# Kernel optimization log

Hardware: AMD Instinct MI355X
Metric: run time of the kernel (lower is better)

Reference implementation:

```python
import jax, jax.numpy as jnp
import numpy as np

B, C, IC, H, W = 4, 64, 32, 128, 128


def _conv1x1(x, w, b):
    # x: [b,c,h,w], w: [o,c], b: [o]
    return jnp.einsum('bchw,oc->bohw', x, w) + b[None, :, None, None]


def _maxpool2(x):
    b, c, h, w = x.shape
    return x.reshape(b, c, h // 2, 2, w // 2, 2).max(axis=(3, 5))


def setup_inputs() -> dict:
    key = jax.random.key(0)
    ks = jax.random.split(key, 11)
    sc = 0.05
    return {
        'target': jax.random.normal(ks[0], (B, C, H, W), jnp.float32),
        'ref': jax.random.normal(ks[1], (B, C, H, W), jnp.float32),
        'ref_align': jax.random.normal(ks[2], (B, C, H, W), jnp.float32),
        'theta_w': jax.random.normal(ks[3], (IC, C), jnp.float32) * sc,
        'theta_b': jax.random.normal(ks[4], (IC,), jnp.float32) * sc,
        'phi_w': jax.random.normal(ks[5], (IC, C), jnp.float32) * sc,
        'phi_b': jax.random.normal(ks[6], (IC,), jnp.float32) * sc,
        'g_w': jax.random.normal(ks[7], (IC, C), jnp.float32) * sc,
        'g_b': jax.random.normal(ks[8], (IC,), jnp.float32) * sc,
        'W_w': jax.random.normal(ks[9], (C, IC), jnp.float32) * sc,
        'W_b': jax.random.normal(ks[10], (C,), jnp.float32) * sc,
    }


def reference(target, ref, ref_align, theta_w, theta_b, phi_w, phi_b, g_w, g_b, W_w, W_b):
    b, c, h, w = target.shape
    N = h * w
    # phi, g: 1x1 conv then 2x2 maxpool -> [b, ic, N/4]
    phi = _maxpool2(_conv1x1(ref, phi_w, phi_b)).reshape(b, -1, N // 4)
    g = _maxpool2(_conv1x1(ref_align, g_w, g_b)).reshape(b, -1, N // 4)
    theta = _conv1x1(target, theta_w, theta_b).reshape(b, -1, N)  # [b, ic, N]
    # softmax-free attention: s [b, N, N/4]
    s = jnp.einsum('bin,bim->bnm', theta, phi) / N
    y = jnp.einsum('bnm,bim->bin', s, g)  # [b, ic, N]
    y = y.reshape(b, -1, h, w)
    return _conv1x1(y, W_w, W_b) + target
```

## Files before the change

### kernel.cpp

```cpp
#include <hip/hip_runtime.h>

#define Bn  4
#define Cc  64
#define ICc 32
#define Hh  128
#define Ww  128
#define Nn  (Hh*Ww)
#define Hp  (Hh/2)
#define Wp  (Ww/2)
#define Mm  (Hp*Wp)
#define Sg  4

__global__ __launch_bounds__(256) void conv_pool_kernel(
    const float* __restrict__ ref, const float* __restrict__ ref_align,
    const float* __restrict__ phi_w, const float* __restrict__ phi_b,
    const float* __restrict__ g_w,   const float* __restrict__ g_b,
    float* __restrict__ P, float* __restrict__ G)
{
    const int z   = blockIdx.z;
    const int inp = z & 1;
    const int ich = (z >> 1) * 16;
    const float* in   = inp ? ref_align : ref;
    const float* wmat = (inp ? g_w : phi_w) + ich * Cc;
    const float* bias = (inp ? g_b : phi_b) + ich;
    float* outp       = inp ? G : P;

    __shared__ float sw[16 * Cc];
    __shared__ float sb[16];
    for (int idx = threadIdx.x; idx < 16 * Cc; idx += 256) sw[idx] = wmat[idx];
    if (threadIdx.x < 16) sb[threadIdx.x] = bias[threadIdx.x];
    __syncthreads();

    const int icq = (threadIdx.x >> 7) * 8;
    const int t   = threadIdx.x & 127;
    const int pw  = t >> 1;
    const int r   = t & 1;
    const int ph  = blockIdx.x;
    const int b   = blockIdx.y;
    const int hh  = 2 * ph + r;

    const float2* xrow = (const float2*)(in + ((size_t)b * Cc * Hh + hh) * Ww);
    const int cs2 = (Hh * Ww) / 2;

    float acc0[8], acc1[8];
    #pragma unroll
    for (int i = 0; i < 8; ++i) { acc0[i] = sb[icq + i]; acc1[i] = sb[icq + i]; }

    #pragma unroll 8
    for (int c = 0; c < Cc; ++c) {
        float2 v = xrow[c * cs2 + pw];
        #pragma unroll
        for (int i = 0; i < 8; ++i) {
            float w = sw[(icq + i) * Cc + c];
            acc0[i] = fmaf(w, v.x, acc0[i]);
            acc1[i] = fmaf(w, v.y, acc1[i]);
        }
    }

    const int m = ph * Wp + pw;
    #pragma unroll
    for (int i = 0; i < 8; ++i) {
        float mx = fmaxf(acc0[i], acc1[i]);
        mx = fmaxf(mx, __shfl_xor(mx, 1, 64));
        if (r == 0) outp[((size_t)(b * ICc + ich + icq + i)) * Mm + m] = mx;
    }
}

__global__ __launch_bounds__(256) void gram_kernel(
    const float* __restrict__ P, const float* __restrict__ G,
    float* __restrict__ Apart)
{
    const int i = blockIdx.x, b = blockIdx.y, s = blockIdx.z;
    const int cm4 = Mm / 4;
    const int q   = s * 256 + threadIdx.x;
    const float4* G4 = (const float4*)(G + (size_t)b * ICc * Mm);
    const float4* P4 = (const float4*)(P + (size_t)b * ICc * Mm);

    const float4 g = G4[i * cm4 + q];

    float acc[ICc];
    #pragma unroll 8
    for (int j = 0; j < ICc; ++j) {
        float4 p = P4[j * cm4 + q];
        acc[j] = fmaf(g.x, p.x, fmaf(g.y, p.y, fmaf(g.z, p.z, g.w * p.w)));
    }

    #pragma unroll
    for (int j = 0; j < ICc; ++j) {
        #pragma unroll
        for (int off = 32; off > 0; off >>= 1)
            acc[j] += __shfl_xor(acc[j], off, 64);
    }

    __shared__ float red[4][ICc];
    const int lane = threadIdx.x & 63, wid = threadIdx.x >> 6;
    if (lane == 0)
        for (int j = 0; j < ICc; ++j) red[wid][j] = acc[j];
    __syncthreads();

    if (threadIdx.x < ICc) {
        float sum = red[0][threadIdx.x] + red[1][threadIdx.x]
                  + red[2][threadIdx.x] + red[3][threadIdx.x];
        Apart[(((size_t)b * Sg + s) * ICc + i) * ICc + threadIdx.x] = sum;
    }
}

__global__ __launch_bounds__(256) void apply_kernel(
    const float* __restrict__ x, const float* __restrict__ Apart,
    const float* __restrict__ theta_w, const float* __restrict__ theta_b,
    const float* __restrict__ W_w,     const float* __restrict__ W_b,
    float* __restrict__ out)
{
    const int b  = blockIdx.y;
    const int ob = blockIdx.z * 8;

    __shared__ float sA[ICc * ICc];
    __shared__ float sT[8 * ICc];
    __shared__ float sM[8 * Cc];
    __shared__ float sv[8];

    const float* Ab = Apart + (size_t)b * Sg * ICc * ICc;
    for (int idx = threadIdx.x; idx < ICc * ICc; idx += 256) {
        float s = 0.f;
        #pragma unroll
        for (int k = 0; k < Sg; ++k) s += Ab[k * ICc * ICc + idx];
        sA[idx] = s;
    }
    __syncthreads();

    {
        const int ol = threadIdx.x >> 5, j = threadIdx.x & 31;
        const float* wr = W_w + (ob + ol) * ICc;
        float t = 0.f;
        #pragma unroll
        for (int i = 0; i < ICc; ++i) t = fmaf(wr[i], sA[i * ICc + j], t);
        sT[ol * ICc + j] = t;
    }
    __syncthreads();

    const float invN = 1.f / (float)Nn;
    for (int idx = threadIdx.x; idx < 8 * Cc; idx += 256) {
        const int ol = idx >> 6, c = idx & 63;
        float s = 0.f;
        #pragma unroll
        for (int j = 0; j < ICc; ++j) s = fmaf(sT[ol * ICc + j], theta_w[j * Cc + c], s);
        sM[idx] = s * invN + ((ob + ol) == c ? 1.f : 0.f);
    }
    if (threadIdx.x < 8) {
        float v = 0.f;
        #pragma unroll
        for (int j = 0; j < ICc; ++j) v = fmaf(sT[threadIdx.x * ICc + j], theta_b[j], v);
        sv[threadIdx.x] = v * invN + W_b[ob + threadIdx.x];
    }
    __syncthreads();

    const int n2 = blockIdx.x * 256 + threadIdx.x;
    const float2* xb  = (const float2*)(x + (size_t)b * Cc * Nn);
    float2*       ob2 = (float2*)(out + (size_t)b * Cc * Nn);

    float ax[8], ay[8];
    #pragma unroll
    for (int i = 0; i < 8; ++i) { ax[i] = sv[i]; ay[i] = sv[i]; }

    #pragma unroll 8
    for (int c = 0; c < Cc; ++c) {
        float2 xv = xb[c * (Nn / 2) + n2];
        #pragma unroll
        for (int i = 0; i < 8; ++i) {
            float w = sM[i * Cc + c];
            ax[i] = fmaf(w, xv.x, ax[i]);
            ay[i] = fmaf(w, xv.y, ay[i]);
        }
    }

    #pragma unroll
    for (int i = 0; i < 8; ++i) {
        float2 o2; o2.x = ax[i]; o2.y = ay[i];
        ob2[(ob + i) * (Nn / 2) + n2] = o2;
    }
}

extern "C" void kernel_launch(void* const* d_in, const int* in_sizes, int n_in,
                              void* d_out, int out_size, void* d_ws, size_t ws_size,
                              hipStream_t stream) {
    const float* target    = (const float*)d_in[0];
    const float* ref       = (const float*)d_in[1];
    const float* ref_align = (const float*)d_in[2];
    const float* theta_w   = (const float*)d_in[3];
    const float* theta_b   = (const float*)d_in[4];
    const float* phi_w     = (const float*)d_in[5];
    const float* phi_b     = (const float*)d_in[6];
    const float* g_w       = (const float*)d_in[7];
    const float* g_b       = (const float*)d_in[8];
    const float* W_w       = (const float*)d_in[9];
    const float* W_b       = (const float*)d_in[10];
    float* out = (float*)d_out;

    float* ws    = (float*)d_ws;
    float* P     = ws;
    float* G     = P + (size_t)Bn * ICc * Mm;
    float* Apart = G + (size_t)Bn * ICc * Mm;

    conv_pool_kernel<<<dim3(Hp, Bn, 4), 256, 0, stream>>>(ref, ref_align,
                                                          phi_w, phi_b, g_w, g_b, P, G);
    gram_kernel<<<dim3(ICc, Bn, Sg), 256, 0, stream>>>(P, G, Apart);
    apply_kernel<<<dim3(Nn / 512, Bn, 8), 256, 0, stream>>>(target, Apart,
                                                            theta_w, theta_b,
                                                            W_w, W_b, out);
}
```

Before: 147.6 us.

## Fuse conv+maxpool with Gram reduction via shared-memory tiles and atomics

Merges the phi/g conv-pool kernel with the Gram kernel. Each block now computes all 32 output channels for both inputs on one pooled row, keeps the pooled tiles in LDS, and accumulates the 32x32 Gram partial with atomicAdd into a zeroed buffer. This removes the P/G global round trip and one launch, at the cost of 64 accumulator registers per thread, fewer blocks (256), many atomics, and non-deterministic summation order.

```diff
diff --git a/kernel.cpp b/kernel.cpp
--- a/kernel.cpp
+++ b/kernel.cpp
@@ -9,104 +9,96 @@
 #define Hp  (Hh/2)
 #define Wp  (Ww/2)
 #define Mm  (Hp*Wp)
-#define Sg  4
+#define PAD 66
 
-__global__ __launch_bounds__(256) void conv_pool_kernel(
+__global__ __launch_bounds__(256) void zero_A(float* __restrict__ A)
+{
+    ((float4*)A)[blockIdx.x * 256 + threadIdx.x] = make_float4(0.f, 0.f, 0.f, 0.f);
+}
+
+__global__ __launch_bounds__(256) void conv_gram_kernel(
     const float* __restrict__ ref, const float* __restrict__ ref_align,
     const float* __restrict__ phi_w, const float* __restrict__ phi_b,
     const float* __restrict__ g_w,   const float* __restrict__ g_b,
-    float* __restrict__ P, float* __restrict__ G)
+    float* __restrict__ A)
 {
-    const int z   = blockIdx.z;
-    const int inp = z & 1;
-    const int ich = (z >> 1) * 16;
-    const float* in   = inp ? ref_align : ref;
-    const float* wmat = (inp ? g_w : phi_w) + ich * Cc;
-    const float* bias = (inp ? g_b : phi_b) + ich;
-    float* outp       = inp ? G : P;
+    __shared__ float swT[2][Cc * ICc];
+    __shared__ float sb[2][ICc];
+    __shared__ float tile[2][ICc][PAD];
 
-    __shared__ float sw[16 * Cc];
-    __shared__ float sb[16];
-    for (int idx = threadIdx.x; idx < 16 * Cc; idx += 256) sw[idx] = wmat[idx];
-    if (threadIdx.x < 16) sb[threadIdx.x] = bias[threadIdx.x];
+    const int b = blockIdx.y, ph = blockIdx.x, tid = threadIdx.x;
+
+    for (int idx = tid; idx < Cc * ICc; idx += 256) {
+        const int c = idx >> 5, i = idx & 31;
+        swT[0][idx] = phi_w[i * Cc + c];
+        swT[1][idx] = g_w[i * Cc + c];
+    }
+    if (tid < ICc) { sb[0][tid] = phi_b[tid]; sb[1][tid] = g_b[tid]; }
     __syncthreads();
 
-    const int icq = (threadIdx.x >> 7) * 8;
-    const int t   = threadIdx.x & 127;
-    const int pw  = t >> 1;
-    const int r   = t & 1;
-    const int ph  = blockIdx.x;
-    const int b   = blockIdx.y;
-    const int hh  = 2 * ph + r;
+    const int r   = tid & 1;
+    const int img = (tid >> 1) & 1;
+    const int pw  = tid >> 2;
+    const float* in = img ? ref_align : ref;
+    const float2* xrow = (const float2*)in
+                       + ((size_t)(b * Cc * Hh) + 2 * ph + r) * (Ww / 2);
+    const int cs2 = (Hh * Ww) / 2;
+    const float* wimg = swT[img];
 
-    const float2* xrow = (const float2*)(in + ((size_t)b * Cc * Hh + hh) * Ww);
-    const int cs2 = (Hh * Ww) / 2;
+    float acc0[ICc], acc1[ICc];
+    #pragma unroll
+    for (int i = 0; i < ICc; ++i) { acc0[i] = sb[img][i]; acc1[i] = sb[img][i]; }
 
-    float acc0[8], acc1[8];
-    #pragma unroll
-    for (int i = 0; i < 8; ++i) { acc0[i] = sb[icq + i]; acc1[i] = sb[icq + i]; }
-
-    #pragma unroll 8
+    #pragma unroll 4
     for (int c = 0; c < Cc; ++c) {
-        float2 v = xrow[c * cs2 + pw];
+        const float2 v = xrow[c * cs2 + pw];
+        const float4* w4 = (const float4*)(wimg + c * ICc);
         #pragma unroll
-        for (int i = 0; i < 8; ++i) {
-            float w = sw[(icq + i) * Cc + c];
-            acc0[i] = fmaf(w, v.x, acc0[i]);
-            acc1[i] = fmaf(w, v.y, acc1[i]);
+        for (int q = 0; q < 8; ++q) {
+            const float4 w = w4[q];
+            acc0[4*q+0] = fmaf(w.x, v.x, acc0[4*q+0]);
+            acc1[4*q+0] = fmaf(w.x, v.y, acc1[4*q+0]);
+            acc0[4*q+1] = fmaf(w.y, v.x, acc0[4*q+1]);
+            acc1[4*q+1] = fmaf(w.y, v.y, acc1[4*q+1]);
+            acc0[4*q+2] = fmaf(w.z, v.x, acc0[4*q+2]);
+            acc1[4*q+2] = fmaf(w.z, v.y, acc1[4*q+2]);
+            acc0[4*q+3] = fmaf(w.w, v.x, acc0[4*q+3]);
+            acc1[4*q+3] = fmaf(w.w, v.y, acc1[4*q+3]);
         }
     }
 
-    const int m = ph * Wp + pw;
     #pragma unroll
-    for (int i = 0; i < 8; ++i) {
+    for (int i = 0; i < ICc; ++i) {
         float mx = fmaxf(acc0[i], acc1[i]);
         mx = fmaxf(mx, __shfl_xor(mx, 1, 64));
-        if (r == 0) outp[((size_t)(b * ICc + ich + icq + i)) * Mm + m] = mx;
+        if (r == 0) tile[img][i][pw] = mx;
     }
-}
-
-__global__ __launch_bounds__(256) void gram_kernel(
-    const float* __restrict__ P, const float* __restrict__ G,
-    float* __restrict__ Apart)
-{
-    const int i = blockIdx.x, b = blockIdx.y, s = blockIdx.z;
-    const int cm4 = Mm / 4;
-    const int q   = s * 256 + threadIdx.x;
-    const float4* G4 = (const float4*)(G + (size_t)b * ICc * Mm);
-    const float4* P4 = (const float4*)(P + (size_t)b * ICc * Mm);
-
-    const float4 g = G4[i * cm4 + q];
-
-    float acc[ICc];
-    #pragma unroll 8
-    for (int j = 0; j < ICc; ++j) {
-        float4 p = P4[j * cm4 + q];
-        acc[j] = fmaf(g.x, p.x, fmaf(g.y, p.y, fmaf(g.z, p.z, g.w * p.w)));
-    }
-
-    #pragma unroll
-    for (int j = 0; j < ICc; ++j) {
-        #pragma unroll
-        for (int off = 32; off > 0; off >>= 1)
-            acc[j] += __shfl_xor(acc[j], off, 64);
-    }
-
-    __shared__ float red[4][ICc];
-    const int lane = threadIdx.x & 63, wid = threadIdx.x >> 6;
-    if (lane == 0)
-        for (int j = 0; j < ICc; ++j) red[wid][j] = acc[j];
     __syncthreads();
 
-    if (threadIdx.x < ICc) {
-        float sum = red[0][threadIdx.x] + red[1][threadIdx.x]
-                  + red[2][threadIdx.x] + red[3][threadIdx.x];
-        Apart[(((size_t)b * Sg + s) * ICc + i) * ICc + threadIdx.x] = sum;
+    const int i  = tid >> 3;
+    const int j0 = (tid & 7) * 4;
+    float s0 = 0.f, s1 = 0.f, s2 = 0.f, s3 = 0.f;
+    #pragma unroll 8
+    for (int p = 0; p < Wp / 2; ++p) {
+        const float2 gv = *(const float2*)&tile[1][i][2 * p];
+        const float2 p0 = *(const float2*)&tile[0][j0 + 0][2 * p];
+        const float2 p1 = *(const float2*)&tile[0][j0 + 1][2 * p];
+        const float2 p2 = *(const float2*)&tile[0][j0 + 2][2 * p];
+        const float2 p3 = *(const float2*)&tile[0][j0 + 3][2 * p];
+        s0 = fmaf(gv.x, p0.x, fmaf(gv.y, p0.y, s0));
+        s1 = fmaf(gv.x, p1.x, fmaf(gv.y, p1.y, s1));
+        s2 = fmaf(gv.x, p2.x, fmaf(gv.y, p2.y, s2));
+        s3 = fmaf(gv.x, p3.x, fmaf(gv.y, p3.y, s3));
     }
+    float* Ab = A + ((size_t)b * ICc + i) * ICc + j0;
+    atomicAdd(Ab + 0, s0);
+    atomicAdd(Ab + 1, s1);
+    atomicAdd(Ab + 2, s2);
+    atomicAdd(Ab + 3, s3);
 }
 
 __global__ __launch_bounds__(256) void apply_kernel(
-    const float* __restrict__ x, const float* __restrict__ Apart,
+    const float* __restrict__ x, const float* __restrict__ A,
     const float* __restrict__ theta_w, const float* __restrict__ theta_b,
     const float* __restrict__ W_w,     const float* __restrict__ W_b,
     float* __restrict__ out)
@@ -119,13 +111,8 @@
     __shared__ float sM[8 * Cc];
     __shared__ float sv[8];
 
-    const float* Ab = Apart + (size_t)b * Sg * ICc * ICc;
-    for (int idx = threadIdx.x; idx < ICc * ICc; idx += 256) {
-        float s = 0.f;
-        #pragma unroll
-        for (int k = 0; k < Sg; ++k) s += Ab[k * ICc * ICc + idx];
-        sA[idx] = s;
-    }
+    for (int idx = threadIdx.x; idx < ICc * ICc; idx += 256)
+        sA[idx] = A[(size_t)b * ICc * ICc + idx];
     __syncthreads();
 
     {
@@ -196,15 +183,12 @@
     const float* W_b       = (const float*)d_in[10];
     float* out = (float*)d_out;
 
-    float* ws    = (float*)d_ws;
-    float* P     = ws;
-    float* G     = P + (size_t)Bn * ICc * Mm;
-    float* Apart = G + (size_t)Bn * ICc * Mm;
+    float* A = (float*)d_ws;
 
-    conv_pool_kernel<<<dim3(Hp, Bn, 4), 256, 0, stream>>>(ref, ref_align,
-                                                          phi_w, phi_b, g_w, g_b, P, G);
-    gram_kernel<<<dim3(ICc, Bn, Sg), 256, 0, stream>>>(P, G, Apart);
-    apply_kernel<<<dim3(Nn / 512, Bn, 8), 256, 0, stream>>>(target, Apart,
+    zero_A<<<4, 256, 0, stream>>>(A);
+    conv_gram_kernel<<<dim3(Hp, Bn), 256, 0, stream>>>(ref, ref_align,
+                                                       phi_w, phi_b, g_w, g_b, A);
+    apply_kernel<<<dim3(Nn / 512, Bn, 8), 256, 0, stream>>>(target, A,
                                                             theta_w, theta_b,
                                                             W_w, W_b, out);
 }
```

Measured after the change: 156.0 us. +5.7%, slower.
